# Kernel tuning notes

Measured on AMD Instinct MI355X. Metric: run time of the kernel, lower is better.

Reference implementation:

```python
import jax, jax.numpy as jnp
import numpy as np

B, N, EM = 16, 1024, 768
D_K, D_V, H = 768, 768, 12

def setup_inputs() -> dict:
    key = jax.random.key(0)
    ks = jax.random.split(key, 4)
    s = 0.02
    x = jax.random.normal(ks[0], (B, N, EM), dtype=jnp.float32)
    W_qk = jax.random.normal(ks[1], (EM, 2 * D_K), dtype=jnp.float32) * s
    b_qk = jnp.zeros((2 * D_K,), dtype=jnp.float32)
    W_v = jax.random.normal(ks[2], (EM, D_V), dtype=jnp.float32) * s
    b_v = jnp.zeros((D_V,), dtype=jnp.float32)
    W_proj = jax.random.normal(ks[3], (D_V, EM), dtype=jnp.float32) * s
    b_proj = jnp.zeros((EM,), dtype=jnp.float32)
    return {"x": x, "W_qk": W_qk, "b_qk": b_qk, "W_v": W_v, "b_v": b_v,
            "W_proj": W_proj, "b_proj": b_proj}

def reference(x, W_qk, b_qk, W_v, b_v, W_proj, b_proj):
    b, n, _ = x.shape
    d = D_K // H  # per-head dim
    # qk Linear -> [B,N,2*d_K]; rearrange 'b n (h d qk) -> qk b h n d'
    # i.e. last dim splits as (h, d, 2) with qk fastest-varying.
    qk = (x @ W_qk + b_qk).reshape(b, n, H, d, 2)
    Q = jnp.transpose(qk[..., 0], (0, 2, 1, 3))  # [B,H,N,d]
    K = jnp.transpose(qk[..., 1], (0, 2, 1, 3))  # [B,H,N,d]
    V = (x @ W_v + b_v).reshape(b, n, H, D_V // H).transpose(0, 2, 1, 3)  # [B,H,N,dv]
    scores = jnp.einsum('bhqd,bhkd->bhqk', Q, K) / jnp.sqrt(jnp.float32(d))
    att = jax.nn.softmax(scores, axis=-1)  # dropout p=0 -> identity
    out = jnp.einsum('bhqk,bhkv->bhqv', att, V)  # [B,H,N,dv]
    out = out.transpose(0, 2, 1, 3).reshape(b, n, D_V)
    return out @ W_proj + b_proj
```

## Files before the change

kernel.cpp:

```cpp
#include <hip/hip_runtime.h>
#include <hip/hip_bf16.h>
#include <stdint.h>

typedef unsigned short u16;
typedef __bf16 bf16_t;
typedef bf16_t bf16x8 __attribute__((ext_vector_type(8)));
typedef short s16x4 __attribute__((ext_vector_type(4)));
typedef float f32x4 __attribute__((ext_vector_type(4)));

__device__ __forceinline__ u16 f2bf(float f) {
    union { float f; uint32_t i; } v; v.f = f;
    uint32_t i = v.i;
    uint32_t r = (i + 0x7FFFu + ((i >> 16) & 1u)) >> 16;
    return (u16)r;
}

__device__ __forceinline__ void gload_lds16(const u16* g, u16* l) {
    auto gp = (const __attribute__((address_space(1))) void*)g;
    auto lp = (__attribute__((address_space(3))) void*)(uintptr_t)l;
    __builtin_amdgcn_global_load_lds(gp, lp, 16, 0, 0);
}

__global__ void convert_f32_bf16_kernel(const float* __restrict__ src,
                                        u16* __restrict__ dst, int n4) {
    int i = blockIdx.x * blockDim.x + threadIdx.x;
    if (i < n4) {
        float4 v = ((const float4*)src)[i];
        ushort4 o;
        o.x = f2bf(v.x); o.y = f2bf(v.y); o.z = f2bf(v.z); o.w = f2bf(v.w);
        ((ushort4*)dst)[i] = o;
    }
}

__global__ void transpose_qk_kernel(const float* __restrict__ W, const float* __restrict__ b,
                                    u16* __restrict__ Wt, float* __restrict__ bp) {
    int r = blockIdx.x;
    int qk = (r >= 768) ? 1 : 0;
    int hd = r - qk * 768;
    int c = (hd >> 6) * 128 + (hd & 63) * 2 + qk;
    float s = qk ? 1.0f : 0.125f;
    for (int k = threadIdx.x; k < 768; k += 256)
        Wt[r * 768 + k] = f2bf(s * W[k * 1536 + c]);
    if (threadIdx.x == 0) bp[r] = s * b[c];
}

__global__ void transpose_sq_kernel(const float* __restrict__ W, u16* __restrict__ Wt) {
    int n = blockIdx.x;
    for (int k = threadIdx.x; k < 768; k += 256)
        Wt[n * 768 + k] = f2bf(W[k * 768 + n]);
}

template<int MODE>
__global__ __launch_bounds__(256)
void gemm_bt_kernel(const u16* __restrict__ A, const u16* __restrict__ Bt,
                    const float* __restrict__ bias, void* __restrict__ Cout,
                    void* __restrict__ Cout2, int M, int N, int K) {
    __shared__ __attribute__((aligned(16))) u16 As[128 * 64];
    __shared__ __attribute__((aligned(16))) u16 Bs[128 * 64];

    const int tid  = threadIdx.x;
    const int lane = tid & 63;
    const int wave = tid >> 6;
    const int l16  = lane & 15;
    const int quad = lane >> 4;
    const int m0 = blockIdx.y * 128;
    const int n0 = blockIdx.x * 128;
    const int wm = (wave & 1) * 64;
    const int wn = (wave >> 1) * 64;

    f32x4 acc[4][4];
#pragma unroll
    for (int i = 0; i < 4; i++)
#pragma unroll
        for (int j = 0; j < 4; j++) acc[i][j] = (f32x4){0.f, 0.f, 0.f, 0.f};

    const int rs   = lane >> 3;
    const int gseg = (lane & 7) ^ rs;
    const u16* Ag[4]; const u16* Bg[4];
#pragma unroll
    for (int c = 0; c < 4; c++) {
        Ag[c] = A  + (size_t)(m0 + c * 32 + wave * 8 + rs) * K + gseg * 8;
        Bg[c] = Bt + (size_t)(n0 + c * 32 + wave * 8 + rs) * K + gseg * 8;
    }
    u16* AsW = As + wave * 512;
    u16* BsW = Bs + wave * 512;
    const int sw7 = l16 & 7;

    for (int k0 = 0; k0 < K; k0 += 64) {
#pragma unroll
        for (int c = 0; c < 4; c++) {
            gload_lds16(Ag[c] + k0, AsW + c * 2048);
            gload_lds16(Bg[c] + k0, BsW + c * 2048);
        }
        __syncthreads();

        bf16x8 af[4][2], bfr[4][2];
#pragma unroll
        for (int i = 0; i < 4; i++) {
#pragma unroll
            for (int h = 0; h < 2; h++) {
                af[i][h]  = *(const bf16x8*)&As[(wm + i * 16 + l16) * 64 +
                                                (((h * 4 + quad) ^ sw7) * 8)];
                bfr[i][h] = *(const bf16x8*)&Bs[(wn + i * 16 + l16) * 64 +
                                                (((h * 4 + quad) ^ sw7) * 8)];
            }
        }
#pragma unroll
        for (int i = 0; i < 4; i++)
#pragma unroll
            for (int j = 0; j < 4; j++) {
#pragma unroll
                for (int h = 0; h < 2; h++) {
                    if constexpr (MODE == 3)
                        acc[i][j] = __builtin_amdgcn_mfma_f32_16x16x32_bf16(af[i][h], bfr[j][h], acc[i][j], 0, 0, 0);
                    else
                        acc[i][j] = __builtin_amdgcn_mfma_f32_16x16x32_bf16(bfr[j][h], af[i][h], acc[i][j], 0, 0, 0);
                }
            }
        __syncthreads();
    }

    if constexpr (MODE == 3) {
#pragma unroll
        for (int j = 0; j < 4; j++) {
            int cnb = n0 + wn + j * 16;
            int h   = cnb >> 6;
            int dv  = (cnb & 63) + l16;
            float bv = bias[cnb + l16];
#pragma unroll
            for (int i = 0; i < 4; i++) {
                int cm = m0 + wm + i * 16 + quad * 4;
                int bb = cm >> 10, n = cm & 1023;
                ushort4 o;
                o.x = f2bf(acc[i][j][0] + bv);
                o.y = f2bf(acc[i][j][1] + bv);
                o.z = f2bf(acc[i][j][2] + bv);
                o.w = f2bf(acc[i][j][3] + bv);
                *(ushort4*)&((u16*)Cout)[((size_t)((bb * 12 + h) * 64 + dv)) * 1024 + n] = o;
            }
        }
    } else {
#pragma unroll
        for (int j = 0; j < 4; j++) {
            int f0 = n0 + wn + j * 16 + quad * 4;
            float4 bv = *(const float4*)&bias[f0];
            if constexpr (MODE == 2) {
                int qk = f0 >= 768;
                int hd = f0 - qk * 768;
                int h  = hd >> 6;
                int d0 = hd & 63;
                u16* dst = (u16*)(qk ? Cout2 : Cout);
#pragma unroll
                for (int i = 0; i < 4; i++) {
                    int t = m0 + wm + i * 16 + l16;
                    int bb = t >> 10, n = t & 1023;
                    ushort4 o;
                    o.x = f2bf(acc[i][j][0] + bv.x);
                    o.y = f2bf(acc[i][j][1] + bv.y);
                    o.z = f2bf(acc[i][j][2] + bv.z);
                    o.w = f2bf(acc[i][j][3] + bv.w);
                    *(ushort4*)&dst[((size_t)((bb * 12 + h) * 1024 + n)) * 64 + d0] = o;
                }
            } else {
#pragma unroll
                for (int i = 0; i < 4; i++) {
                    int t = m0 + wm + i * 16 + l16;
                    float4 o;
                    o.x = acc[i][j][0] + bv.x;
                    o.y = acc[i][j][1] + bv.y;
                    o.z = acc[i][j][2] + bv.z;
                    o.w = acc[i][j][3] + bv.w;
                    *(float4*)&((float*)Cout)[(size_t)t * N + f0] = o;
                }
            }
        }
    }
}

__global__ __launch_bounds__(512)
void attention_mfma_kernel(const u16* __restrict__ Qp, const u16* __restrict__ Kp,
                           const u16* __restrict__ Vp, u16* __restrict__ attout) {
    __shared__ __attribute__((aligned(16))) u16 Ks[64 * 64];
    __shared__ __attribute__((aligned(16))) u16 Vs[64 * 64];

    const int tid  = threadIdx.x;
    const int wave = tid >> 6;
    const int lane = tid & 63;
    const int l16  = lane & 15;
    const int quad = lane >> 4;
    const int bh = blockIdx.y;
    const int b  = bh / 12, h = bh % 12;
    const int q0 = blockIdx.x * 256 + wave * 32;

    const u16* Qhead = Qp + (size_t)bh * 1024 * 64;
    const u16* Khead = Kp + (size_t)bh * 1024 * 64;
    const u16* Vhead = Vp + (size_t)bh * 64 * 1024;

    bf16x8 qf[2][2];
#pragma unroll
    for (int qb = 0; qb < 2; qb++) {
        const u16* qrow = Qhead + (size_t)(q0 + qb * 16 + l16) * 64;
        qf[qb][0] = *(const bf16x8*)(qrow + quad * 8);
        qf[qb][1] = *(const bf16x8*)(qrow + 32 + quad * 8);
    }

    f32x4 oacc[2][4];
#pragma unroll
    for (int qb = 0; qb < 2; qb++)
#pragma unroll
        for (int db = 0; db < 4; db++) oacc[qb][db] = (f32x4){0.f, 0.f, 0.f, 0.f};
    float l_part[2] = {0.f, 0.f};

    const int srow = tid >> 3;
    const int gseg = (tid & 7) ^ (srow & 7);
    u16* KsW = Ks + wave * 512;
    u16* VsW = Vs + wave * 512;
    const int sw7 = l16 & 7;

    for (int kt = 0; kt < 1024; kt += 64) {
        gload_lds16(Khead + (size_t)(kt + srow) * 64 + gseg * 8, KsW);
        gload_lds16(Vhead + (size_t)srow * 1024 + kt + gseg * 8, VsW);
        __syncthreads();

        union { uint32_t u[4]; bf16x8 v; } pf8[2][2];
        {
            bf16x8 kf[4][2];
#pragma unroll
            for (int jb = 0; jb < 4; jb++) {
#pragma unroll
                for (int hf = 0; hf < 2; hf++)
                    kf[jb][hf] = *(const bf16x8*)&Ks[(jb * 16 + l16) * 64 +
                                                     (((hf * 4 + quad) ^ sw7) * 8)];
            }
#pragma unroll
            for (int qb = 0; qb < 2; qb++) {
#pragma unroll
                for (int jb = 0; jb < 4; jb++) {
                    f32x4 st = (f32x4){0.f, 0.f, 0.f, 0.f};
                    st = __builtin_amdgcn_mfma_f32_16x16x32_bf16(kf[jb][0], qf[qb][0], st, 0, 0, 0);
                    st = __builtin_amdgcn_mfma_f32_16x16x32_bf16(kf[jb][1], qf[qb][1], st, 0, 0, 0);
                    float e0 = __expf(st[0]), e1 = __expf(st[1]);
                    float e2 = __expf(st[2]), e3 = __expf(st[3]);
                    l_part[qb] += (e0 + e1) + (e2 + e3);
                    union { __hip_bfloat162 h2; uint32_t u; } c0, c1;
                    c0.h2 = __float22bfloat162_rn(make_float2(e0, e1));
                    c1.h2 = __float22bfloat162_rn(make_float2(e2, e3));
                    pf8[qb][jb >> 1].u[(jb & 1) * 2 + 0] = c0.u;
                    pf8[qb][jb >> 1].u[(jb & 1) * 2 + 1] = c1.u;
                }
            }
        }

#pragma unroll
        for (int db = 0; db < 4; db++) {
#pragma unroll
            for (int jp = 0; jp < 2; jp++) {
                union { s16x4 h[2]; bf16x8 v; } vb8;
                int glo = 4 * jp + (quad >> 1);
                int ghi = glo + 2;
                vb8.h[0] = *(const s16x4*)&Vs[(db * 16 + l16) * 64 +
                                              ((glo ^ sw7) * 8) + (quad & 1) * 4];
                vb8.h[1] = *(const s16x4*)&Vs[(db * 16 + l16) * 64 +
                                              ((ghi ^ sw7) * 8) + (quad & 1) * 4];
#pragma unroll
                for (int qb = 0; qb < 2; qb++)
                    oacc[qb][db] = __builtin_amdgcn_mfma_f32_16x16x32_bf16(
                        pf8[qb][jp].v, vb8.v, oacc[qb][db], 0, 0, 0);
            }
        }
        __syncthreads();
    }

#pragma unroll
    for (int qb = 0; qb < 2; qb++) {
        float l = l_part[qb];
        l += __shfl_xor(l, 16);
        l += __shfl_xor(l, 32);
        float linv[4];
#pragma unroll
        for (int r = 0; r < 4; r++)
            linv[r] = 1.0f / __shfl(l, quad * 4 + r);
        u16* orow = attout + (size_t)(b * 1024 + q0 + qb * 16 + quad * 4) * 768 + h * 64 + l16;
#pragma unroll
        for (int db = 0; db < 4; db++)
#pragma unroll
            for (int r = 0; r < 4; r++)
                orow[(size_t)r * 768 + db * 16] = f2bf(oacc[qb][db][r] * linv[r]);
    }
}

extern "C" void kernel_launch(void* const* d_in, const int* in_sizes, int n_in,
                              void* d_out, int out_size, void* d_ws, size_t ws_size,
                              hipStream_t stream) {
    const float* x      = (const float*)d_in[0];
    const float* W_qk   = (const float*)d_in[1];
    const float* b_qk   = (const float*)d_in[2];
    const float* W_v    = (const float*)d_in[3];
    const float* b_v    = (const float*)d_in[4];
    const float* W_proj = (const float*)d_in[5];
    const float* b_proj = (const float*)d_in[6];
    float* out = (float*)d_out;

    char* ws = (char*)d_ws;
    size_t off = 0;
    auto alloc = [&](size_t bytes) { void* p = ws + off; off += (bytes + 255) & ~255ull; return p; };
    u16*   xb     = (u16*)alloc((size_t)16384 * 768 * 2);
    u16*   Wqkt   = (u16*)alloc((size_t)1536 * 768 * 2);
    float* bqkp   = (float*)alloc(1536 * 4);
    u16*   Wvt    = (u16*)alloc((size_t)768 * 768 * 2);
    u16*   Wprojt = (u16*)alloc((size_t)768 * 768 * 2);
    u16*   Qp     = (u16*)alloc((size_t)16384 * 768 * 2);
    u16*   Kp     = (u16*)alloc((size_t)16384 * 768 * 2);
    u16*   Vp     = (u16*)alloc((size_t)16384 * 768 * 2);
    u16*   attout = (u16*)alloc((size_t)16384 * 768 * 2);

    convert_f32_bf16_kernel<<<12288, 256, 0, stream>>>(x, xb, 3145728);
    transpose_qk_kernel<<<1536, 256, 0, stream>>>(W_qk, b_qk, Wqkt, bqkp);
    transpose_sq_kernel<<<768, 256, 0, stream>>>(W_v, Wvt);
    transpose_sq_kernel<<<768, 256, 0, stream>>>(W_proj, Wprojt);

    gemm_bt_kernel<2><<<dim3(12, 128), 256, 0, stream>>>(xb, Wqkt, bqkp, Qp, Kp, 16384, 1536, 768);
    gemm_bt_kernel<3><<<dim3(6, 128), 256, 0, stream>>>(xb, Wvt, b_v, Vp, nullptr, 16384, 768, 768);
    attention_mfma_kernel<<<dim3(4, 192), 512, 0, stream>>>(Qp, Kp, Vp, attout);
    gemm_bt_kernel<1><<<dim3(6, 128), 256, 0, stream>>>(attout, Wprojt, b_proj, out, nullptr, 16384, 768, 768);
}
```

Baseline: 349.3 us.

## Double-buffer attention K/V tiles, add XCD-aware block swizzle and MFMA priority

```diff
diff --git a/kernel.cpp b/kernel.cpp
--- a/kernel.cpp
+++ b/kernel.cpp
@@ -63,8 +63,11 @@
     const int wave = tid >> 6;
     const int l16  = lane & 15;
     const int quad = lane >> 4;
-    const int m0 = blockIdx.y * 128;
-    const int n0 = blockIdx.x * 128;
+    const int nxt = N >> 7;
+    const int cpx = (int)gridDim.x >> 3;
+    const int swz = ((int)blockIdx.x & 7) * cpx + ((int)blockIdx.x >> 3);
+    const int m0 = (swz / nxt) * 128;
+    const int n0 = (swz % nxt) * 128;
     const int wm = (wave & 1) * 64;
     const int wn = (wave >> 1) * 64;
 
@@ -180,17 +183,19 @@
 __global__ __launch_bounds__(512)
 void attention_mfma_kernel(const u16* __restrict__ Qp, const u16* __restrict__ Kp,
                            const u16* __restrict__ Vp, u16* __restrict__ attout) {
-    __shared__ __attribute__((aligned(16))) u16 Ks[64 * 64];
-    __shared__ __attribute__((aligned(16))) u16 Vs[64 * 64];
+    __shared__ __attribute__((aligned(16))) u16 Ks[2][64 * 64];
+    __shared__ __attribute__((aligned(16))) u16 Vs[2][64 * 64];
 
     const int tid  = threadIdx.x;
     const int wave = tid >> 6;
     const int lane = tid & 63;
     const int l16  = lane & 15;
     const int quad = lane >> 4;
-    const int bh = blockIdx.y;
-    const int b  = bh / 12, h = bh % 12;
-    const int q0 = blockIdx.x * 256 + wave * 32;
+    const int flat = blockIdx.x;
+    const int swz  = (flat & 7) * 96 + (flat >> 3);
+    const int bh   = swz >> 2;
+    const int b    = bh / 12, h = bh % 12;
+    const int q0   = (swz & 3) * 256 + wave * 32;
 
     const u16* Qhead = Qp + (size_t)bh * 1024 * 64;
     const u16* Khead = Kp + (size_t)bh * 1024 * 64;
@@ -213,14 +218,22 @@
 
     const int srow = tid >> 3;
     const int gseg = (tid & 7) ^ (srow & 7);
-    u16* KsW = Ks + wave * 512;
-    u16* VsW = Vs + wave * 512;
+    const u16* Kg = Khead + (size_t)srow * 64 + gseg * 8;
+    const u16* Vg = Vhead + (size_t)srow * 1024 + gseg * 8;
     const int sw7 = l16 & 7;
 
-    for (int kt = 0; kt < 1024; kt += 64) {
-        gload_lds16(Khead + (size_t)(kt + srow) * 64 + gseg * 8, KsW);
-        gload_lds16(Vhead + (size_t)srow * 1024 + kt + gseg * 8, VsW);
+    gload_lds16(Kg, &Ks[0][wave * 512]);
+    gload_lds16(Vg, &Vs[0][wave * 512]);
+
+    int cur = 0;
+    for (int t = 0; t < 16; ++t) {
         __syncthreads();
+        if (t < 15) {
+            gload_lds16(Kg + (t + 1) * 4096, &Ks[cur ^ 1][wave * 512]);
+            gload_lds16(Vg + (t + 1) * 64,   &Vs[cur ^ 1][wave * 512]);
+        }
+        const u16* Ksc = Ks[cur];
+        const u16* Vsc = Vs[cur];
 
         union { uint32_t u[4]; bf16x8 v; } pf8[2][2];
         {
@@ -229,16 +242,18 @@
             for (int jb = 0; jb < 4; jb++) {
 #pragma unroll
                 for (int hf = 0; hf < 2; hf++)
-                    kf[jb][hf] = *(const bf16x8*)&Ks[(jb * 16 + l16) * 64 +
-                                                     (((hf * 4 + quad) ^ sw7) * 8)];
+                    kf[jb][hf] = *(const bf16x8*)&Ksc[(jb * 16 + l16) * 64 +
+                                                      (((hf * 4 + quad) ^ sw7) * 8)];
             }
 #pragma unroll
             for (int qb = 0; qb < 2; qb++) {
 #pragma unroll
                 for (int jb = 0; jb < 4; jb++) {
                     f32x4 st = (f32x4){0.f, 0.f, 0.f, 0.f};
+                    __builtin_amdgcn_s_setprio(1);
                     st = __builtin_amdgcn_mfma_f32_16x16x32_bf16(kf[jb][0], qf[qb][0], st, 0, 0, 0);
                     st = __builtin_amdgcn_mfma_f32_16x16x32_bf16(kf[jb][1], qf[qb][1], st, 0, 0, 0);
+                    __builtin_amdgcn_s_setprio(0);
                     float e0 = __expf(st[0]), e1 = __expf(st[1]);
                     float e2 = __expf(st[2]), e3 = __expf(st[3]);
                     l_part[qb] += (e0 + e1) + (e2 + e3);
@@ -251,6 +266,7 @@
             }
         }
 
+        __builtin_amdgcn_s_setprio(1);
 #pragma unroll
         for (int db = 0; db < 4; db++) {
 #pragma unroll
@@ -258,17 +274,18 @@
                 union { s16x4 h[2]; bf16x8 v; } vb8;
                 int glo = 4 * jp + (quad >> 1);
                 int ghi = glo + 2;
-                vb8.h[0] = *(const s16x4*)&Vs[(db * 16 + l16) * 64 +
-                                              ((glo ^ sw7) * 8) + (quad & 1) * 4];
-                vb8.h[1] = *(const s16x4*)&Vs[(db * 16 + l16) * 64 +
-                                              ((ghi ^ sw7) * 8) + (quad & 1) * 4];
+                vb8.h[0] = *(const s16x4*)&Vsc[(db * 16 + l16) * 64 +
+                                               ((glo ^ sw7) * 8) + (quad & 1) * 4];
+                vb8.h[1] = *(const s16x4*)&Vsc[(db * 16 + l16) * 64 +
+                                               ((ghi ^ sw7) * 8) + (quad & 1) * 4];
 #pragma unroll
                 for (int qb = 0; qb < 2; qb++)
                     oacc[qb][db] = __builtin_amdgcn_mfma_f32_16x16x32_bf16(
                         pf8[qb][jp].v, vb8.v, oacc[qb][db], 0, 0, 0);
             }
         }
-        __syncthreads();
+        __builtin_amdgcn_s_setprio(0);
+        cur ^= 1;
     }
 
 #pragma unroll
@@ -319,8 +336,8 @@
     transpose_sq_kernel<<<768, 256, 0, stream>>>(W_v, Wvt);
     transpose_sq_kernel<<<768, 256, 0, stream>>>(W_proj, Wprojt);
 
-    gemm_bt_kernel<2><<<dim3(12, 128), 256, 0, stream>>>(xb, Wqkt, bqkp, Qp, Kp, 16384, 1536, 768);
-    gemm_bt_kernel<3><<<dim3(6, 128), 256, 0, stream>>>(xb, Wvt, b_v, Vp, nullptr, 16384, 768, 768);
-    attention_mfma_kernel<<<dim3(4, 192), 512, 0, stream>>>(Qp, Kp, Vp, attout);
-    gemm_bt_kernel<1><<<dim3(6, 128), 256, 0, stream>>>(attout, Wprojt, b_proj, out, nullptr, 16384, 768, 768);
-}
+    gemm_bt_kernel<2><<<1536, 256, 0, stream>>>(xb, Wqkt, bqkp, Qp, Kp, 16384, 1536, 768);
+    gemm_bt_kernel<3><<<768, 256, 0, stream>>>(xb, Wvt, b_v, Vp, nullptr, 16384, 768, 768);
+    attention_mfma_kernel<<<768, 512, 0, stream>>>(Qp, Kp, Vp, attout);
+    gemm_bt_kernel<1><<<768, 256, 0, stream>>>(attout, Wprojt, b_proj, out, nullptr, 16384, 768, 768);
+}
```

After: 326.2 us. 6.6% less time.
